# Kernel optimization log

Hardware: AMD Instinct MI355X
Metric: run time of the kernel (lower is better)

The kernel has to match this reference:

```python
import jax, jax.numpy as jnp
import numpy as np
from jax import lax

H = 1028  # hidden_size


def _lstm_layer(x, w_ih, w_hh, b_ih, b_hh):
    # x: [B, T, in], w_ih: [4H, in], w_hh: [4H, H] (PyTorch gate order i,f,g,o)
    B, T, _ = x.shape
    h_dim = w_hh.shape[1]
    # Precompute input contribution for all timesteps (memory-bound GEMM)
    xg = jnp.einsum('bti,gi->btg', x, w_ih) + b_ih + b_hh  # [B, T, 4H]

    def step(carry, xt):
        h, c = carry
        g = xt + h @ w_hh.T  # [B, 4H]
        i, f, gg, o = jnp.split(g, 4, axis=-1)
        i = jax.nn.sigmoid(i)
        f = jax.nn.sigmoid(f)
        gg = jnp.tanh(gg)
        o = jax.nn.sigmoid(o)
        c = f * c + i * gg
        h = o * jnp.tanh(c)
        return (h, c), h

    h0 = jnp.zeros((B, h_dim), x.dtype)
    c0 = jnp.zeros((B, h_dim), x.dtype)
    _, hs = lax.scan(step, (h0, c0), jnp.swapaxes(xg, 0, 1))  # [T, B, H]
    return jnp.swapaxes(hs, 0, 1)  # [B, T, H]


def setup_inputs() -> dict:
    key = jax.random.key(0)
    ks = jax.random.split(key, 12)
    s = 1.0 / np.sqrt(H)  # torch LSTM/Linear init scale

    def u(k, shape):
        return jax.random.uniform(k, shape, jnp.float32, -s, s)

    x = jax.random.normal(ks[0], (1, 16384, 1), dtype=jnp.float32)
    return {
        'x': x,
        'w_ih0': u(ks[1], (4 * H, 1)),
        'w_hh0': u(ks[2], (4 * H, H)),
        'b_ih0': u(ks[3], (4 * H,)),
        'b_hh0': u(ks[4], (4 * H,)),
        'w_ih1': u(ks[5], (4 * H, H)),
        'w_hh1': u(ks[6], (4 * H, H)),
        'b_ih1': u(ks[7], (4 * H,)),
        'b_hh1': u(ks[8], (4 * H,)),
        'lin_w': u(ks[9], (1, H)),
        'lin_b': u(ks[10], (1,)),
    }


def reference(x, w_ih0, w_hh0, b_ih0, b_hh0, w_ih1, w_hh1, b_ih1, b_hh1, lin_w, lin_b):
    h1 = _lstm_layer(x, w_ih0, w_hh0, b_ih0, b_hh0)   # [B, T, H]
    h2 = _lstm_layer(h1, w_ih1, w_hh1, b_ih1, b_hh1)  # [B, T, H]
    return h2 @ lin_w.T + lin_b                        # [B, T, 1]
```

## Files before the change

kernel.cpp:

```cpp
#include <hip/hip_runtime.h>
#include <math.h>

#define HH    1028
#define TT    16384
#define UP    1056
#define HSU   1056
#define HS    1056
#define NWG0  66
#define NWG1  132
#define NWGT  (NWG0 + NWG1)
#define R0    1024
#define R0M   (R0 - 1)
#define R1M   15

typedef unsigned long long u64;
typedef unsigned int uint4v __attribute__((ext_vector_type(4)));

__device__ __forceinline__ u64 ld_u64(const u64* p) {
    return __hip_atomic_load(p, __ATOMIC_RELAXED, __HIP_MEMORY_SCOPE_AGENT);
}
__device__ __forceinline__ void st_u64(u64* p, u64 v) {
    __hip_atomic_store(p, v, __ATOMIC_RELAXED, __HIP_MEMORY_SCOPE_AGENT);
}
__device__ __forceinline__ unsigned ld_u32(const unsigned* p) {
    return __hip_atomic_load(p, __ATOMIC_RELAXED, __HIP_MEMORY_SCOPE_AGENT);
}
__device__ __forceinline__ void st_u32(unsigned* p, unsigned v) {
    __hip_atomic_store(p, v, __ATOMIC_RELAXED, __HIP_MEMORY_SCOPE_AGENT);
}
__device__ __forceinline__ float sigmf(float x) { return 1.0f / (1.0f + expf(-x)); }
__device__ __forceinline__ u64 pack(unsigned tag, float v) {
    return ((u64)tag << 32) | (u64)__float_as_uint(v);
}

#define POLL16(dst, ptr) \
    asm volatile("global_load_dwordx4 %0, %1, off sc0 sc1" : "=v"(dst) : "v"(ptr))

__device__ __forceinline__ void stage132w(const u64* __restrict__ src, float* __restrict__ lds,
                                          int base, int lane, unsigned want, long long& budget) {
    const u64* p0 = src + base + 2 * lane;
    const u64* p1 = src + base + 2 * (64 + lane);
    bool d0 = false, d1 = (lane >= 2);
    uint4v r0 = {0, 0, 0, 0}, r1 = {0, 0, 0, 0};
    int spin = 2;
    for (;;) {
        if (!d0) POLL16(r0, p0);
        if (!d1) POLL16(r1, p1);
        asm volatile("s_waitcnt vmcnt(0)" ::: "memory");
        __builtin_amdgcn_sched_barrier(0);
        if (!d0 && r0[1] == want && r0[3] == want) {
            *(float2*)&lds[base + 2 * lane] =
                make_float2(__uint_as_float(r0[0]), __uint_as_float(r0[2]));
            d0 = true;
        }
        if (!d1 && r1[1] == want && r1[3] == want) {
            *(float2*)&lds[base + 2 * (64 + lane)] =
                make_float2(__uint_as_float(r1[0]), __uint_as_float(r1[2]));
            d1 = true;
        }
        if (__all(d0 & d1)) break;
        if (--budget < 0) break;
        if (spin > 0) { --spin; continue; }
        __builtin_amdgcn_s_sleep(1);
    }
}

__device__ __forceinline__ void stage264w(const u64* __restrict__ src, float* __restrict__ lds,
                                          int base, int lane, unsigned want, long long& budget) {
    const u64* p0 = src + base + 2 * lane;
    const u64* p1 = src + base + 2 * (64 + lane);
    const u64* p2 = src + base + 2 * (128 + lane);
    bool d0 = false, d1 = false, d2 = (lane >= 4);
    uint4v r0 = {0, 0, 0, 0}, r1 = {0, 0, 0, 0}, r2 = {0, 0, 0, 0};
    int spin = 2;
    for (;;) {
        if (!d0) POLL16(r0, p0);
        if (!d1) POLL16(r1, p1);
        if (!d2) POLL16(r2, p2);
        asm volatile("s_waitcnt vmcnt(0)" ::: "memory");
        __builtin_amdgcn_sched_barrier(0);
        if (!d0 && r0[1] == want && r0[3] == want) {
            *(float2*)&lds[base + 2 * lane] =
                make_float2(__uint_as_float(r0[0]), __uint_as_float(r0[2]));
            d0 = true;
        }
        if (!d1 && r1[1] == want && r1[3] == want) {
            *(float2*)&lds[base + 2 * (64 + lane)] =
                make_float2(__uint_as_float(r1[0]), __uint_as_float(r1[2]));
            d1 = true;
        }
        if (!d2 && r2[1] == want && r2[3] == want) {
            *(float2*)&lds[base + 2 * (128 + lane)] =
                make_float2(__uint_as_float(r2[0]), __uint_as_float(r2[2]));
            d2 = true;
        }
        if (__all(d0 & d1 & d2)) break;
        if (--budget < 0) break;
        if (spin > 0) { --spin; continue; }
        __builtin_amdgcn_s_sleep(1);
    }
}

__global__ __launch_bounds__(1024, 4) void wn_fused(
    const float* __restrict__ x,
    const float* __restrict__ w_ih0, const float* __restrict__ w_hh0,
    const float* __restrict__ b_ih0, const float* __restrict__ b_hh0,
    const float* __restrict__ w_ih1, const float* __restrict__ w_hh1,
    const float* __restrict__ b_ih1, const float* __restrict__ b_hh1,
    u64* __restrict__ ring0,
    u64* __restrict__ ring1,
    float* __restrict__ h2hist,
    unsigned* __restrict__ l1prog)
{
    __shared__ float smem[4 * UP + 128];
    const int tid  = threadIdx.x;
    const int lane = tid & 63;
    const int w    = tid >> 6;

    for (int i = tid; i < 4 * UP + 128; i += 1024) smem[i] = 0.0f;

    if (blockIdx.x < NWG0) {
        float* hbuf = smem;
        float* gbuf = smem + 2 * UP;
        const int wg   = blockIdx.x;
        const int row  = tid >> 4;
        const int k0   = tid & 15;
        const int gate = row >> 4;
        const int du   = row & 15;
        const int u    = wg * 16 + du;
        const bool real = (u < HH);
        const int wr   = gate * HH + (real ? u : 0);

        float wv[16][4], wt0 = 0.f, wt1 = 0.f;
#pragma unroll
        for (int m = 0; m < 16; ++m) {
            const int j = k0 * 4 + m * 64;
#pragma unroll
            for (int q = 0; q < 4; ++q)
                wv[m][q] = (real && j + q < HH) ? w_hh0[(size_t)wr * HH + j + q] : 0.0f;
        }
        {   const int j = 1024 + k0 * 2;
            wt0 = (real && j     < HH) ? w_hh0[(size_t)wr * HH + j]     : 0.0f;
            wt1 = (real && j + 1 < HH) ? w_hh0[(size_t)wr * HH + j + 1] : 0.0f; }
#pragma unroll
        for (int m = 0; m < 16; ++m)
#pragma unroll
            for (int q = 0; q < 4; ++q) asm volatile("" : "+v"(wv[m][q]));
        asm volatile("" : "+v"(wt0), "+v"(wt1));

        const float wx = real ? w_ih0[wr] : 0.0f;
        const float bs = real ? (b_ih0[wr] + b_hh0[wr]) : 0.0f;
        __syncthreads();

        long long budget = 20000000LL;
        float c_reg = 0.0f;
        for (int t = 0; t < TT; ++t) {
            if (t > 0) {
                if (w == 0) {
                    const float* gl = gbuf + ((t - 1) & 1) * 64;
                    if (lane < 16) {
                        const float gi = gl[lane], gf = gl[16 + lane];
                        const float gg = gl[32 + lane], go = gl[48 + lane];
                        const float iv = sigmf(gi), fv = sigmf(gf), gv = tanhf(gg), ov = sigmf(go);
                        c_reg = fv * c_reg + iv * gv;
                        float hv = ov * tanhf(c_reg);
                        if (wg * 16 + lane >= HH) hv = 0.0f;
                        st_u64(ring0 + (size_t)((t - 1) & R0M) * HSU + wg * 16 + lane,
                               pack((unsigned)t, hv));
                    }
                } else if (w >= 4 && w < 12) {
                    stage132w(ring0 + (size_t)((t - 1) & R0M) * HSU, hbuf + (t & 1) * UP,
                              (w - 4) * 132, lane, (unsigned)t, budget);
                } else if (w == 1 && lane == 0 && (t & 255) == 0) {
                    for (;;) {
                        unsigned p = ld_u32(l1prog);
                        if ((int)t - (int)p < R0 - 256) break;
                        if (--budget < 0) break;
                        __builtin_amdgcn_s_sleep(32);
                    }
                }
            }
            __syncthreads();
            const float* hb = hbuf + (t & 1) * UP;
            float acc = 0.0f;
#pragma unroll
            for (int m = 0; m < 16; ++m) {
                const float4 hv = *(const float4*)&hb[k0 * 4 + m * 64];
                acc = fmaf(wv[m][0], hv.x, acc);
                acc = fmaf(wv[m][1], hv.y, acc);
                acc = fmaf(wv[m][2], hv.z, acc);
                acc = fmaf(wv[m][3], hv.w, acc);
            }
            {   const float2 hv = *(const float2*)&hb[1024 + k0 * 2];
                acc = fmaf(wt0, hv.x, acc);
                acc = fmaf(wt1, hv.y, acc); }
#pragma unroll
            for (int off = 1; off < 16; off <<= 1) acc += __shfl_xor(acc, off);
            if (k0 == 0) gbuf[(t & 1) * 64 + row] = acc + x[t] * wx + bs;
            __syncthreads();
        }
        if (w == 0 && lane < 16) {
            const float* gl = gbuf + ((TT - 1) & 1) * 64;
            const float gi = gl[lane], gf = gl[16 + lane];
            const float gg = gl[32 + lane], go = gl[48 + lane];
            const float iv = sigmf(gi), fv = sigmf(gf), gv = tanhf(gg), ov = sigmf(go);
            c_reg = fv * c_reg + iv * gv;
            float hv = ov * tanhf(c_reg);
            if (wg * 16 + lane >= HH) hv = 0.0f;
            st_u64(ring0 + (size_t)((TT - 1) & R0M) * HSU + wg * 16 + lane,
                   pack((unsigned)TT, hv));
        }
    } else {
        float* abuf = smem;
        float* bbuf = smem + 2 * UP;
        float* gbuf = smem + 4 * UP;
        const int wg   = blockIdx.x - NWG0;
        const int row  = tid >> 5;
        const int k0   = tid & 31;
        const int gate = row >> 3;
        const int du   = row & 7;
        const int u    = wg * 8 + du;
        const bool real = (u < HH);
        const int wr   = gate * HH + (real ? u : 0);

        float wiv[8][4], whv[8][4], wit = 0.f, wht = 0.f;
#pragma unroll
        for (int m = 0; m < 8; ++m) {
            const int j = k0 * 4 + m * 128;
#pragma unroll
            for (int q = 0; q < 4; ++q) {
                const bool inb = real && (j + q < HH);
                wiv[m][q] = inb ? w_ih1[(size_t)wr * HH + j + q] : 0.0f;
                whv[m][q] = inb ? w_hh1[(size_t)wr * HH + j + q] : 0.0f;
            }
        }
        {   const int j = 1024 + k0;
            wit = (real && j < HH) ? w_ih1[(size_t)wr * HH + j] : 0.0f;
            wht = (real && j < HH) ? w_hh1[(size_t)wr * HH + j] : 0.0f; }
#pragma unroll
        for (int m = 0; m < 8; ++m)
#pragma unroll
            for (int q = 0; q < 4; ++q) {
                asm volatile("" : "+v"(wiv[m][q]));
                asm volatile("" : "+v"(whv[m][q]));
            }
        asm volatile("" : "+v"(wit), "+v"(wht));
        const float bs = real ? (b_ih1[wr] + b_hh1[wr]) : 0.0f;
        __syncthreads();

        long long budget = 20000000LL;
        float c_reg = 0.0f;
        for (int t = 0; t < TT; ++t) {
            if (w == 0) {
                if (t > 0) {
                    const float* gl = gbuf + ((t - 1) & 1) * 32;
                    if (lane < 8) {
                        const float gi = gl[lane], gf = gl[8 + lane];
                        const float gg = gl[16 + lane], go = gl[24 + lane];
                        const float iv = sigmf(gi), fv = sigmf(gf), gv = tanhf(gg), ov = sigmf(go);
                        c_reg = fv * c_reg + iv * gv;
                        float hv = ov * tanhf(c_reg);
                        if (wg * 8 + lane >= HH) hv = 0.0f;
                        st_u64(ring1 + (size_t)((t - 1) & R1M) * HSU + wg * 8 + lane,
                               pack((unsigned)t, hv));
                        h2hist[(size_t)(t - 1) * HS + wg * 8 + lane] = hv;
                    }
                }
            } else if (w >= 4 && w < 12) {
                if (t > 0)
                    stage132w(ring1 + (size_t)((t - 1) & R1M) * HSU, bbuf + (t & 1) * UP,
                              (w - 4) * 132, lane, (unsigned)t, budget);
            } else if (w >= 12) {
                stage264w(ring0 + (size_t)(t & R0M) * HSU, abuf + (t & 1) * UP,
                          (w - 12) * 264, lane, (unsigned)(t + 1), budget);
            }
            __syncthreads();
            const float* ab = abuf + (t & 1) * UP;
            const float* bb = bbuf + (t & 1) * UP;
            float acc = 0.0f;
#pragma unroll
            for (int m = 0; m < 8; ++m) {
                const float4 ha = *(const float4*)&ab[k0 * 4 + m * 128];
                const float4 hb2 = *(const float4*)&bb[k0 * 4 + m * 128];
                acc = fmaf(wiv[m][0], ha.x, acc);
                acc = fmaf(wiv[m][1], ha.y, acc);
                acc = fmaf(wiv[m][2], ha.z, acc);
                acc = fmaf(wiv[m][3], ha.w, acc);
                acc = fmaf(whv[m][0], hb2.x, acc);
                acc = fmaf(whv[m][1], hb2.y, acc);
                acc = fmaf(whv[m][2], hb2.z, acc);
                acc = fmaf(whv[m][3], hb2.w, acc);
            }
            acc = fmaf(wit, ab[1024 + k0], acc);
            acc = fmaf(wht, bb[1024 + k0], acc);
#pragma unroll
            for (int off = 1; off < 32; off <<= 1) acc += __shfl_xor(acc, off);
            if (k0 == 0) gbuf[(t & 1) * 32 + row] = acc + bs;
            __syncthreads();
            if (w == 1 && lane == 0 && wg == 0 && (t & 255) == 255)
                st_u32(l1prog, (unsigned)(t + 1));
        }
        if (w == 0 && lane < 8) {
            const float* gl = gbuf + ((TT - 1) & 1) * 32;
            const float gi = gl[lane], gf = gl[8 + lane];
            const float gg = gl[16 + lane], go = gl[24 + lane];
            const float iv = sigmf(gi), fv = sigmf(gf), gv = tanhf(gg), ov = sigmf(go);
            c_reg = fv * c_reg + iv * gv;
            float hv = ov * tanhf(c_reg);
            if (wg * 8 + lane >= HH) hv = 0.0f;
            h2hist[(size_t)(TT - 1) * HS + wg * 8 + lane] = hv;
        }
    }
}

__global__ __launch_bounds__(256) void wn_proj(
    const float* __restrict__ h2,
    const float* __restrict__ lin_w,
    const float* __restrict__ lin_b,
    float* __restrict__ out)
{
    const int lane = threadIdx.x & 63;
    const int wv   = threadIdx.x >> 6;
    const int t    = blockIdx.x * 4 + wv;
    const float* hp = h2 + (size_t)t * HS;
    float acc = 0.0f;
#pragma unroll
    for (int m = 0; m < 4; ++m) {
        const int j = lane * 4 + m * 256;
        const float4 h4 = *(const float4*)(hp + j);
        const float4 w4 = *(const float4*)(lin_w + j);
        acc += h4.x * w4.x + h4.y * w4.y + h4.z * w4.z + h4.w * w4.w;
    }
    if (lane == 0) {
#pragma unroll
        for (int j = 1024; j < HH; ++j) acc += hp[j] * lin_w[j];
    }
#pragma unroll
    for (int off = 1; off < 64; off <<= 1) acc += __shfl_xor(acc, off);
    if (lane == 0) out[t] = acc + lin_b[0];
}

extern "C" void kernel_launch(void* const* d_in, const int* in_sizes, int n_in,
                              void* d_out, int out_size, void* d_ws, size_t ws_size,
                              hipStream_t stream) {
    const float* x     = (const float*)d_in[0];
    const float* w_ih0 = (const float*)d_in[1];
    const float* w_hh0 = (const float*)d_in[2];
    const float* b_ih0 = (const float*)d_in[3];
    const float* b_hh0 = (const float*)d_in[4];
    const float* w_ih1 = (const float*)d_in[5];
    const float* w_hh1 = (const float*)d_in[6];
    const float* b_ih1 = (const float*)d_in[7];
    const float* b_hh1 = (const float*)d_in[8];
    const float* lin_w = (const float*)d_in[9];
    const float* lin_b = (const float*)d_in[10];
    float* out = (float*)d_out;

    char* ws = (char*)d_ws;
    const size_t R0B = (size_t)R0 * HSU * 8;
    const size_t R1B = (size_t)16 * HSU * 8;
    const size_t H2B = (size_t)TT * HS * 4;
    u64* ring0 = (u64*)(ws);
    u64* ring1 = (u64*)(ws + R0B);
    float* h2hist = (float*)(ws + R0B + R1B);
    unsigned* l1prog = (unsigned*)(ws + R0B + R1B + H2B);

    wn_fused<<<NWGT, 1024, 0, stream>>>(x, w_ih0, w_hh0, b_ih0, b_hh0,
                                        w_ih1, w_hh1, b_ih1, b_hh1,
                                        ring0, ring1, h2hist, l1prog);
    wn_proj<<<TT / 4, 256, 0, stream>>>(h2hist, lin_w, lin_b, out);
}
```

Before: 42.34 ms.

## Give each wave one hidden unit, compute gates in-wave, cut per-step barriers

Restructures both LSTM layers so each wave owns one hidden unit and holds all four gate rows of weights in registers. The wave reduces its dot products with a full-wave shuffle and applies the gate nonlinearities itself, which removes the separate gate buffer and the second barrier per timestep. Per-unit results are packed with a step tag into LDS slots and collected by wave 0, which publishes them to the global ring. Every wave then helps poll the next step's hidden state, so the loop needs one __syncthreads per step instead of two. The cost is more weight registers per lane, a full 64-lane shuffle reduction per gate, and an LDS spin-wait on the critical path.

```diff
diff --git a/kernel.cpp b/kernel.cpp
--- a/kernel.cpp
+++ b/kernel.cpp
@@ -28,6 +28,12 @@
 __device__ __forceinline__ void st_u32(unsigned* p, unsigned v) {
     __hip_atomic_store(p, v, __ATOMIC_RELAXED, __HIP_MEMORY_SCOPE_AGENT);
 }
+__device__ __forceinline__ u64 ld_lds_u64(const u64* p) {
+    return __hip_atomic_load(p, __ATOMIC_RELAXED, __HIP_MEMORY_SCOPE_WORKGROUP);
+}
+__device__ __forceinline__ void st_lds_u64(u64* p, u64 v) {
+    __hip_atomic_store(p, v, __ATOMIC_RELAXED, __HIP_MEMORY_SCOPE_WORKGROUP);
+}
 __device__ __forceinline__ float sigmf(float x) { return 1.0f / (1.0f + expf(-x)); }
 __device__ __forceinline__ u64 pack(unsigned tag, float v) {
     return ((u64)tag << 32) | (u64)__float_as_uint(v);
@@ -36,16 +42,14 @@
 #define POLL16(dst, ptr) \
     asm volatile("global_load_dwordx4 %0, %1, off sc0 sc1" : "=v"(dst) : "v"(ptr))
 
-__device__ __forceinline__ void stage132w(const u64* __restrict__ src, float* __restrict__ lds,
-                                          int base, int lane, unsigned want, long long& budget) {
+__device__ __forceinline__ void stage66w(const u64* __restrict__ src, float* __restrict__ lds,
+                                         int base, int lane, unsigned want, long long& budget) {
     const u64* p0 = src + base + 2 * lane;
-    const u64* p1 = src + base + 2 * (64 + lane);
-    bool d0 = false, d1 = (lane >= 2);
-    uint4v r0 = {0, 0, 0, 0}, r1 = {0, 0, 0, 0};
+    bool d0 = (lane >= 33);
+    uint4v r0 = {0, 0, 0, 0};
     int spin = 2;
     for (;;) {
         if (!d0) POLL16(r0, p0);
-        if (!d1) POLL16(r1, p1);
         asm volatile("s_waitcnt vmcnt(0)" ::: "memory");
         __builtin_amdgcn_sched_barrier(0);
         if (!d0 && r0[1] == want && r0[3] == want) {
@@ -53,12 +57,7 @@
                 make_float2(__uint_as_float(r0[0]), __uint_as_float(r0[2]));
             d0 = true;
         }
-        if (!d1 && r1[1] == want && r1[3] == want) {
-            *(float2*)&lds[base + 2 * (64 + lane)] =
-                make_float2(__uint_as_float(r1[0]), __uint_as_float(r1[2]));
-            d1 = true;
-        }
-        if (__all(d0 & d1)) break;
+        if (__all(d0)) break;
         if (--budget < 0) break;
         if (spin > 0) { --spin; continue; }
         __builtin_amdgcn_s_sleep(1);
@@ -112,203 +111,239 @@
     float* __restrict__ h2hist,
     unsigned* __restrict__ l1prog)
 {
-    __shared__ float smem[4 * UP + 128];
+    __shared__ float smem[4 * UP + 64];
     const int tid  = threadIdx.x;
     const int lane = tid & 63;
     const int w    = tid >> 6;
 
-    for (int i = tid; i < 4 * UP + 128; i += 1024) smem[i] = 0.0f;
+    for (int i = tid; i < 4 * UP + 64; i += 1024) smem[i] = 0.0f;
 
     if (blockIdx.x < NWG0) {
         float* hbuf = smem;
-        float* gbuf = smem + 2 * UP;
+        u64*   pbuf = (u64*)(smem + 4 * UP);
         const int wg   = blockIdx.x;
-        const int row  = tid >> 4;
-        const int k0   = tid & 15;
-        const int gate = row >> 4;
-        const int du   = row & 15;
-        const int u    = wg * 16 + du;
+        const int u    = wg * 16 + w;
         const bool real = (u < HH);
-        const int wr   = gate * HH + (real ? u : 0);
-
-        float wv[16][4], wt0 = 0.f, wt1 = 0.f;
-#pragma unroll
-        for (int m = 0; m < 16; ++m) {
-            const int j = k0 * 4 + m * 64;
-#pragma unroll
-            for (int q = 0; q < 4; ++q)
-                wv[m][q] = (real && j + q < HH) ? w_hh0[(size_t)wr * HH + j + q] : 0.0f;
-        }
-        {   const int j = 1024 + k0 * 2;
-            wt0 = (real && j     < HH) ? w_hh0[(size_t)wr * HH + j]     : 0.0f;
-            wt1 = (real && j + 1 < HH) ? w_hh0[(size_t)wr * HH + j + 1] : 0.0f; }
-#pragma unroll
-        for (int m = 0; m < 16; ++m)
-#pragma unroll
-            for (int q = 0; q < 4; ++q) asm volatile("" : "+v"(wv[m][q]));
-        asm volatile("" : "+v"(wt0), "+v"(wt1));
-
-        const float wx = real ? w_ih0[wr] : 0.0f;
-        const float bs = real ? (b_ih0[wr] + b_hh0[wr]) : 0.0f;
+
+        float wv[4][4][4];
+        float wt[4][4];
+        float wx[4], bsg[4];
+#pragma unroll
+        for (int g = 0; g < 4; ++g) {
+            const int wr = g * HH + (real ? u : 0);
+#pragma unroll
+            for (int m = 0; m < 4; ++m) {
+                const int j = lane * 4 + m * 256;
+#pragma unroll
+                for (int q = 0; q < 4; ++q)
+                    wv[g][m][q] = real ? w_hh0[(size_t)wr * HH + j + q] : 0.0f;
+            }
+#pragma unroll
+            for (int q = 0; q < 4; ++q) {
+                const int j = 1024 + lane * 4 + q;
+                wt[g][q] = (real && lane < 8 && j < HH) ? w_hh0[(size_t)wr * HH + j] : 0.0f;
+            }
+            wx[g]  = real ? w_ih0[wr] : 0.0f;
+            bsg[g] = real ? (b_ih0[wr] + b_hh0[wr]) : 0.0f;
+        }
+#pragma unroll
+        for (int g = 0; g < 4; ++g)
+#pragma unroll
+            for (int m = 0; m < 4; ++m)
+#pragma unroll
+                for (int q = 0; q < 4; ++q) asm volatile("" : "+v"(wv[g][m][q]));
         __syncthreads();
 
         long long budget = 20000000LL;
         float c_reg = 0.0f;
         for (int t = 0; t < TT; ++t) {
-            if (t > 0) {
-                if (w == 0) {
-                    const float* gl = gbuf + ((t - 1) & 1) * 64;
-                    if (lane < 16) {
-                        const float gi = gl[lane], gf = gl[16 + lane];
-                        const float gg = gl[32 + lane], go = gl[48 + lane];
-                        const float iv = sigmf(gi), fv = sigmf(gf), gv = tanhf(gg), ov = sigmf(go);
-                        c_reg = fv * c_reg + iv * gv;
-                        float hv = ov * tanhf(c_reg);
-                        if (wg * 16 + lane >= HH) hv = 0.0f;
-                        st_u64(ring0 + (size_t)((t - 1) & R0M) * HSU + wg * 16 + lane,
-                               pack((unsigned)t, hv));
-                    }
-                } else if (w >= 4 && w < 12) {
-                    stage132w(ring0 + (size_t)((t - 1) & R0M) * HSU, hbuf + (t & 1) * UP,
-                              (w - 4) * 132, lane, (unsigned)t, budget);
-                } else if (w == 1 && lane == 0 && (t & 255) == 0) {
-                    for (;;) {
-                        unsigned p = ld_u32(l1prog);
-                        if ((int)t - (int)p < R0 - 256) break;
-                        if (--budget < 0) break;
-                        __builtin_amdgcn_s_sleep(32);
-                    }
-                }
-            }
-            __syncthreads();
+            const float xt = x[t];
             const float* hb = hbuf + (t & 1) * UP;
-            float acc = 0.0f;
-#pragma unroll
-            for (int m = 0; m < 16; ++m) {
-                const float4 hv = *(const float4*)&hb[k0 * 4 + m * 64];
-                acc = fmaf(wv[m][0], hv.x, acc);
-                acc = fmaf(wv[m][1], hv.y, acc);
-                acc = fmaf(wv[m][2], hv.z, acc);
-                acc = fmaf(wv[m][3], hv.w, acc);
-            }
-            {   const float2 hv = *(const float2*)&hb[1024 + k0 * 2];
-                acc = fmaf(wt0, hv.x, acc);
-                acc = fmaf(wt1, hv.y, acc); }
-#pragma unroll
-            for (int off = 1; off < 16; off <<= 1) acc += __shfl_xor(acc, off);
-            if (k0 == 0) gbuf[(t & 1) * 64 + row] = acc + x[t] * wx + bs;
-            __syncthreads();
-        }
-        if (w == 0 && lane < 16) {
-            const float* gl = gbuf + ((TT - 1) & 1) * 64;
-            const float gi = gl[lane], gf = gl[16 + lane];
-            const float gg = gl[32 + lane], go = gl[48 + lane];
-            const float iv = sigmf(gi), fv = sigmf(gf), gv = tanhf(gg), ov = sigmf(go);
+            float acc[4] = {0.f, 0.f, 0.f, 0.f};
+#pragma unroll
+            for (int m = 0; m < 4; ++m) {
+                const float4 hv4 = *(const float4*)&hb[lane * 4 + m * 256];
+#pragma unroll
+                for (int g = 0; g < 4; ++g) {
+                    acc[g] = fmaf(wv[g][m][0], hv4.x, acc[g]);
+                    acc[g] = fmaf(wv[g][m][1], hv4.y, acc[g]);
+                    acc[g] = fmaf(wv[g][m][2], hv4.z, acc[g]);
+                    acc[g] = fmaf(wv[g][m][3], hv4.w, acc[g]);
+                }
+            }
+            if (lane < 8) {
+                const float4 hv4 = *(const float4*)&hb[1024 + lane * 4];
+#pragma unroll
+                for (int g = 0; g < 4; ++g) {
+                    acc[g] = fmaf(wt[g][0], hv4.x, acc[g]);
+                    acc[g] = fmaf(wt[g][1], hv4.y, acc[g]);
+                    acc[g] = fmaf(wt[g][2], hv4.z, acc[g]);
+                    acc[g] = fmaf(wt[g][3], hv4.w, acc[g]);
+                }
+            }
+#pragma unroll
+            for (int off = 1; off < 64; off <<= 1) {
+#pragma unroll
+                for (int g = 0; g < 4; ++g) acc[g] += __shfl_xor(acc[g], off);
+            }
+#pragma unroll
+            for (int g = 0; g < 4; ++g) acc[g] = fmaf(xt, wx[g], acc[g]) + bsg[g];
+            const float iv = sigmf(acc[0]), fv = sigmf(acc[1]);
+            const float gv = tanhf(acc[2]), ov = sigmf(acc[3]);
             c_reg = fv * c_reg + iv * gv;
             float hv = ov * tanhf(c_reg);
-            if (wg * 16 + lane >= HH) hv = 0.0f;
-            st_u64(ring0 + (size_t)((TT - 1) & R0M) * HSU + wg * 16 + lane,
-                   pack((unsigned)TT, hv));
+            if (!real) hv = 0.0f;
+            if (lane == 0) st_lds_u64(&pbuf[w], pack((unsigned)(t + 1), hv));
+
+            if (w == 0) {
+                const unsigned want = (unsigned)(t + 1);
+                u64 pv = 0; bool d = (lane >= 16);
+                for (;;) {
+                    if (!d) { u64 v2 = ld_lds_u64(&pbuf[lane]);
+                              if ((unsigned)(v2 >> 32) == want) { pv = v2; d = true; } }
+                    if (__all(d)) break;
+                    if (--budget < 0) break;
+                }
+                if (lane < 16)
+                    st_u64(ring0 + (size_t)(t & R0M) * HSU + wg * 16 + lane, pv);
+            } else if (w == 1 && lane == 0 && t > 0 && (t & 255) == 0) {
+                for (;;) {
+                    unsigned p = ld_u32(l1prog);
+                    if ((int)t - (int)p < R0 - 256) break;
+                    if (--budget < 0) break;
+                    __builtin_amdgcn_s_sleep(32);
+                }
+            }
+            if (t + 1 < TT)
+                stage66w(ring0 + (size_t)(t & R0M) * HSU, hbuf + ((t + 1) & 1) * UP,
+                         w * 66, lane, (unsigned)(t + 1), budget);
+            __syncthreads();
         }
     } else {
         float* abuf = smem;
         float* bbuf = smem + 2 * UP;
-        float* gbuf = smem + 4 * UP;
+        u64*   pbuf = (u64*)(smem + 4 * UP);
         const int wg   = blockIdx.x - NWG0;
-        const int row  = tid >> 5;
-        const int k0   = tid & 31;
-        const int gate = row >> 3;
-        const int du   = row & 7;
-        const int u    = wg * 8 + du;
-        const bool real = (u < HH);
-        const int wr   = gate * HH + (real ? u : 0);
-
-        float wiv[8][4], whv[8][4], wit = 0.f, wht = 0.f;
-#pragma unroll
-        for (int m = 0; m < 8; ++m) {
-            const int j = k0 * 4 + m * 128;
-#pragma unroll
-            for (int q = 0; q < 4; ++q) {
-                const bool inb = real && (j + q < HH);
-                wiv[m][q] = inb ? w_ih1[(size_t)wr * HH + j + q] : 0.0f;
-                whv[m][q] = inb ? w_hh1[(size_t)wr * HH + j + q] : 0.0f;
-            }
-        }
-        {   const int j = 1024 + k0;
-            wit = (real && j < HH) ? w_ih1[(size_t)wr * HH + j] : 0.0f;
-            wht = (real && j < HH) ? w_hh1[(size_t)wr * HH + j] : 0.0f; }
-#pragma unroll
-        for (int m = 0; m < 8; ++m)
-#pragma unroll
-            for (int q = 0; q < 4; ++q) {
-                asm volatile("" : "+v"(wiv[m][q]));
-                asm volatile("" : "+v"(whv[m][q]));
-            }
-        asm volatile("" : "+v"(wit), "+v"(wht));
-        const float bs = real ? (b_ih1[wr] + b_hh1[wr]) : 0.0f;
+        const bool comp = (w < 8);
+        const int u    = wg * 8 + (comp ? w : 0);
+        const bool real = comp && (u < HH);
+
+        float wiv[4][4][4], whv[4][4][4];
+        float wti[4][4], wth[4][4], bsg[4];
+        if (comp) {
+#pragma unroll
+            for (int g = 0; g < 4; ++g) {
+                const int wr = g * HH + (real ? u : 0);
+#pragma unroll
+                for (int m = 0; m < 4; ++m) {
+                    const int j = lane * 4 + m * 256;
+#pragma unroll
+                    for (int q = 0; q < 4; ++q) {
+                        wiv[g][m][q] = real ? w_ih1[(size_t)wr * HH + j + q] : 0.0f;
+                        whv[g][m][q] = real ? w_hh1[(size_t)wr * HH + j + q] : 0.0f;
+                    }
+                }
+#pragma unroll
+                for (int q = 0; q < 4; ++q) {
+                    const int j = 1024 + lane * 4 + q;
+                    const bool inb = real && lane < 8 && j < HH;
+                    wti[g][q] = inb ? w_ih1[(size_t)wr * HH + j] : 0.0f;
+                    wth[g][q] = inb ? w_hh1[(size_t)wr * HH + j] : 0.0f;
+                }
+                bsg[g] = real ? (b_ih1[wr] + b_hh1[wr]) : 0.0f;
+            }
+#pragma unroll
+            for (int g = 0; g < 4; ++g)
+#pragma unroll
+                for (int m = 0; m < 4; ++m)
+#pragma unroll
+                    for (int q = 0; q < 4; ++q) {
+                        asm volatile("" : "+v"(wiv[g][m][q]));
+                        asm volatile("" : "+v"(whv[g][m][q]));
+                    }
+        }
+        long long budget = 20000000LL;
+        if (w >= 12)
+            stage264w(ring0, abuf, (w - 12) * 264, lane, 1u, budget);
         __syncthreads();
 
-        long long budget = 20000000LL;
         float c_reg = 0.0f;
         for (int t = 0; t < TT; ++t) {
-            if (w == 0) {
-                if (t > 0) {
-                    const float* gl = gbuf + ((t - 1) & 1) * 32;
+            if (comp) {
+                const float* ab = abuf + (t & 1) * UP;
+                const float* bb = bbuf + (t & 1) * UP;
+                float acc[4] = {0.f, 0.f, 0.f, 0.f};
+#pragma unroll
+                for (int m = 0; m < 4; ++m) {
+                    const float4 ha = *(const float4*)&ab[lane * 4 + m * 256];
+                    const float4 hc = *(const float4*)&bb[lane * 4 + m * 256];
+#pragma unroll
+                    for (int g = 0; g < 4; ++g) {
+                        acc[g] = fmaf(wiv[g][m][0], ha.x, acc[g]);
+                        acc[g] = fmaf(wiv[g][m][1], ha.y, acc[g]);
+                        acc[g] = fmaf(wiv[g][m][2], ha.z, acc[g]);
+                        acc[g] = fmaf(wiv[g][m][3], ha.w, acc[g]);
+                        acc[g] = fmaf(whv[g][m][0], hc.x, acc[g]);
+                        acc[g] = fmaf(whv[g][m][1], hc.y, acc[g]);
+                        acc[g] = fmaf(whv[g][m][2], hc.z, acc[g]);
+                        acc[g] = fmaf(whv[g][m][3], hc.w, acc[g]);
+                    }
+                }
+                if (lane < 8) {
+                    const float4 ha = *(const float4*)&ab[1024 + lane * 4];
+                    const float4 hc = *(const float4*)&bb[1024 + lane * 4];
+#pragma unroll
+                    for (int g = 0; g < 4; ++g) {
+                        acc[g] = fmaf(wti[g][0], ha.x, acc[g]);
+                        acc[g] = fmaf(wti[g][1], ha.y, acc[g]);
+                        acc[g] = fmaf(wti[g][2], ha.z, acc[g]);
+                        acc[g] = fmaf(wti[g][3], ha.w, acc[g]);
+                        acc[g] = fmaf(wth[g][0], hc.x, acc[g]);
+                        acc[g] = fmaf(wth[g][1], hc.y, acc[g]);
+                        acc[g] = fmaf(wth[g][2], hc.z, acc[g]);
+                        acc[g] = fmaf(wth[g][3], hc.w, acc[g]);
+                    }
+                }
+#pragma unroll
+                for (int off = 1; off < 64; off <<= 1) {
+#pragma unroll
+                    for (int g = 0; g < 4; ++g) acc[g] += __shfl_xor(acc[g], off);
+                }
+#pragma unroll
+                for (int g = 0; g < 4; ++g) acc[g] += bsg[g];
+                const float iv = sigmf(acc[0]), fv = sigmf(acc[1]);
+                const float gv = tanhf(acc[2]), ov = sigmf(acc[3]);
+                c_reg = fv * c_reg + iv * gv;
+                float hv = ov * tanhf(c_reg);
+                if (!real) hv = 0.0f;
+                if (lane == 0) st_lds_u64(&pbuf[w], pack((unsigned)(t + 1), hv));
+
+                if (w == 0) {
+                    const unsigned want = (unsigned)(t + 1);
+                    u64 pv = 0; bool d = (lane >= 8);
+                    for (;;) {
+                        if (!d) { u64 v2 = ld_lds_u64(&pbuf[lane]);
+                                  if ((unsigned)(v2 >> 32) == want) { pv = v2; d = true; } }
+                        if (__all(d)) break;
+                        if (--budget < 0) break;
+                    }
                     if (lane < 8) {
-                        const float gi = gl[lane], gf = gl[8 + lane];
-                        const float gg = gl[16 + lane], go = gl[24 + lane];
-                        const float iv = sigmf(gi), fv = sigmf(gf), gv = tanhf(gg), ov = sigmf(go);
-                        c_reg = fv * c_reg + iv * gv;
-                        float hv = ov * tanhf(c_reg);
-                        if (wg * 8 + lane >= HH) hv = 0.0f;
-                        st_u64(ring1 + (size_t)((t - 1) & R1M) * HSU + wg * 8 + lane,
-                               pack((unsigned)t, hv));
-                        h2hist[(size_t)(t - 1) * HS + wg * 8 + lane] = hv;
-                    }
-                }
-            } else if (w >= 4 && w < 12) {
-                if (t > 0)
-                    stage132w(ring1 + (size_t)((t - 1) & R1M) * HSU, bbuf + (t & 1) * UP,
-                              (w - 4) * 132, lane, (unsigned)t, budget);
-            } else if (w >= 12) {
-                stage264w(ring0 + (size_t)(t & R0M) * HSU, abuf + (t & 1) * UP,
-                          (w - 12) * 264, lane, (unsigned)(t + 1), budget);
+                        st_u64(ring1 + (size_t)(t & R1M) * HSU + wg * 8 + lane, pv);
+                        h2hist[(size_t)t * HS + wg * 8 + lane] = __uint_as_float((unsigned)pv);
+                    }
+                } else if (wg == 0 && w == 1 && lane == 0 && (t & 255) == 255) {
+                    st_u32(l1prog, (unsigned)(t + 1));
+                }
+            } else if (w < 12) {
+                if (t + 1 < TT)
+                    stage264w(ring1 + (size_t)(t & R1M) * HSU, bbuf + ((t + 1) & 1) * UP,
+                              (w - 8) * 264, lane, (unsigned)(t + 1), budget);
+            } else {
+                if (t + 1 < TT)
+                    stage264w(ring0 + (size_t)((t + 1) & R0M) * HSU, abuf + ((t + 1) & 1) * UP,
+                              (w - 12) * 264, lane, (unsigned)(t + 2), budget);
             }
             __syncthreads();
-            const float* ab = abuf + (t & 1) * UP;
-            const float* bb = bbuf + (t & 1) * UP;
-            float acc = 0.0f;
-#pragma unroll
-            for (int m = 0; m < 8; ++m) {
-                const float4 ha = *(const float4*)&ab[k0 * 4 + m * 128];
-                const float4 hb2 = *(const float4*)&bb[k0 * 4 + m * 128];
-                acc = fmaf(wiv[m][0], ha.x, acc);
-                acc = fmaf(wiv[m][1], ha.y, acc);
-                acc = fmaf(wiv[m][2], ha.z, acc);
-                acc = fmaf(wiv[m][3], ha.w, acc);
-                acc = fmaf(whv[m][0], hb2.x, acc);
-                acc = fmaf(whv[m][1], hb2.y, acc);
-                acc = fmaf(whv[m][2], hb2.z, acc);
-                acc = fmaf(whv[m][3], hb2.w, acc);
-            }
-            acc = fmaf(wit, ab[1024 + k0], acc);
-            acc = fmaf(wht, bb[1024 + k0], acc);
-#pragma unroll
-            for (int off = 1; off < 32; off <<= 1) acc += __shfl_xor(acc, off);
-            if (k0 == 0) gbuf[(t & 1) * 32 + row] = acc + bs;
-            __syncthreads();
-            if (w == 1 && lane == 0 && wg == 0 && (t & 255) == 255)
-                st_u32(l1prog, (unsigned)(t + 1));
-        }
-        if (w == 0 && lane < 8) {
-            const float* gl = gbuf + ((TT - 1) & 1) * 32;
-            const float gi = gl[lane], gf = gl[8 + lane];
-            const float gg = gl[16 + lane], go = gl[24 + lane];
-            const float iv = sigmf(gi), fv = sigmf(gf), gv = tanhf(gg), ov = sigmf(go);
-            c_reg = fv * c_reg + iv * gv;
-            float hv = ov * tanhf(c_reg);
-            if (wg * 8 + lane >= HH) hv = 0.0f;
-            h2hist[(size_t)(TT - 1) * HS + wg * 8 + lane] = hv;
         }
     }
 }
```

Result: slower. 144.1 ms (+240.4%).

## Halve workgroup size and have each thread compute all four gates of one unit

Applied to the files above, without the earlier changes.

Each workgroup now runs 512 threads instead of 1024. Each thread holds the weights for all four gates of one hidden unit and reuses every loaded h vector across four accumulators. This cuts the number of waves per workgroup and the LDS reads per FMA, which should shorten the per-timestep critical path through __syncthreads. Staging from the rings is spread over fewer, wider waves (176/352 elements each). The cost is more registers per thread, and each wave now has fewer pollers and a longer shuffle reduction.

```diff
diff --git a/kernel.cpp b/kernel.cpp
--- a/kernel.cpp
+++ b/kernel.cpp
@@ -36,11 +36,11 @@
 #define POLL16(dst, ptr) \
     asm volatile("global_load_dwordx4 %0, %1, off sc0 sc1" : "=v"(dst) : "v"(ptr))
 
-__device__ __forceinline__ void stage132w(const u64* __restrict__ src, float* __restrict__ lds,
+__device__ __forceinline__ void stage176w(const u64* __restrict__ src, float* __restrict__ lds,
                                           int base, int lane, unsigned want, long long& budget) {
     const u64* p0 = src + base + 2 * lane;
     const u64* p1 = src + base + 2 * (64 + lane);
-    bool d0 = false, d1 = (lane >= 2);
+    bool d0 = false, d1 = (lane >= 24);
     uint4v r0 = {0, 0, 0, 0}, r1 = {0, 0, 0, 0};
     int spin = 2;
     for (;;) {
@@ -65,12 +65,12 @@
     }
 }
 
-__device__ __forceinline__ void stage264w(const u64* __restrict__ src, float* __restrict__ lds,
+__device__ __forceinline__ void stage352w(const u64* __restrict__ src, float* __restrict__ lds,
                                           int base, int lane, unsigned want, long long& budget) {
     const u64* p0 = src + base + 2 * lane;
     const u64* p1 = src + base + 2 * (64 + lane);
     const u64* p2 = src + base + 2 * (128 + lane);
-    bool d0 = false, d1 = false, d2 = (lane >= 4);
+    bool d0 = false, d1 = false, d2 = (lane >= 48);
     uint4v r0 = {0, 0, 0, 0}, r1 = {0, 0, 0, 0}, r2 = {0, 0, 0, 0};
     int spin = 2;
     for (;;) {
@@ -101,7 +101,7 @@
     }
 }
 
-__global__ __launch_bounds__(1024, 4) void wn_fused(
+__global__ __launch_bounds__(512, 2) void wn_fused(
     const float* __restrict__ x,
     const float* __restrict__ w_ih0, const float* __restrict__ w_hh0,
     const float* __restrict__ b_ih0, const float* __restrict__ b_hh0,
@@ -117,39 +117,40 @@
     const int lane = tid & 63;
     const int w    = tid >> 6;
 
-    for (int i = tid; i < 4 * UP + 128; i += 1024) smem[i] = 0.0f;
+    for (int i = tid; i < 4 * UP + 128; i += 512) smem[i] = 0.0f;
 
     if (blockIdx.x < NWG0) {
         float* hbuf = smem;
         float* gbuf = smem + 2 * UP;
         const int wg   = blockIdx.x;
-        const int row  = tid >> 4;
-        const int k0   = tid & 15;
-        const int gate = row >> 4;
-        const int du   = row & 15;
+        const int hi   = lane >> 5;
+        const int k0   = lane & 31;
+        const int du   = w * 2 + hi;
         const int u    = wg * 16 + du;
         const bool real = (u < HH);
-        const int wr   = gate * HH + (real ? u : 0);
-
-        float wv[16][4], wt0 = 0.f, wt1 = 0.f;
-#pragma unroll
-        for (int m = 0; m < 16; ++m) {
-            const int j = k0 * 4 + m * 64;
-#pragma unroll
-            for (int q = 0; q < 4; ++q)
-                wv[m][q] = (real && j + q < HH) ? w_hh0[(size_t)wr * HH + j + q] : 0.0f;
-        }
-        {   const int j = 1024 + k0 * 2;
-            wt0 = (real && j     < HH) ? w_hh0[(size_t)wr * HH + j]     : 0.0f;
-            wt1 = (real && j + 1 < HH) ? w_hh0[(size_t)wr * HH + j + 1] : 0.0f; }
-#pragma unroll
-        for (int m = 0; m < 16; ++m)
-#pragma unroll
-            for (int q = 0; q < 4; ++q) asm volatile("" : "+v"(wv[m][q]));
-        asm volatile("" : "+v"(wt0), "+v"(wt1));
-
-        const float wx = real ? w_ih0[wr] : 0.0f;
-        const float bs = real ? (b_ih0[wr] + b_hh0[wr]) : 0.0f;
+
+        float wv[4][8][4], wt4[4], wx4[4], bs4[4];
+#pragma unroll
+        for (int g = 0; g < 4; ++g) {
+            const int wr = g * HH + (real ? u : 0);
+#pragma unroll
+            for (int m = 0; m < 8; ++m) {
+                const int j = k0 * 4 + m * 128;
+#pragma unroll
+                for (int q = 0; q < 4; ++q)
+                    wv[g][m][q] = real ? w_hh0[(size_t)wr * HH + j + q] : 0.0f;
+            }
+            const int jt = 1024 + k0;
+            wt4[g] = (real && jt < HH) ? w_hh0[(size_t)wr * HH + jt] : 0.0f;
+            wx4[g] = real ? w_ih0[wr] : 0.0f;
+            bs4[g] = real ? (b_ih0[wr] + b_hh0[wr]) : 0.0f;
+        }
+#pragma unroll
+        for (int g = 0; g < 4; ++g)
+#pragma unroll
+            for (int m = 0; m < 8; ++m)
+#pragma unroll
+                for (int q = 0; q < 4; ++q) asm volatile("" : "+v"(wv[g][m][q]));
         __syncthreads();
 
         long long budget = 20000000LL;
@@ -168,9 +169,9 @@
                         st_u64(ring0 + (size_t)((t - 1) & R0M) * HSU + wg * 16 + lane,
                                pack((unsigned)t, hv));
                     }
-                } else if (w >= 4 && w < 12) {
-                    stage132w(ring0 + (size_t)((t - 1) & R0M) * HSU, hbuf + (t & 1) * UP,
-                              (w - 4) * 132, lane, (unsigned)t, budget);
+                } else if (w >= 2) {
+                    stage176w(ring0 + (size_t)((t - 1) & R0M) * HSU, hbuf + (t & 1) * UP,
+                              (w - 2) * 176, lane, (unsigned)t, budget);
                 } else if (w == 1 && lane == 0 && (t & 255) == 0) {
                     for (;;) {
                         unsigned p = ld_u32(l1prog);
@@ -182,21 +183,33 @@
             }
             __syncthreads();
             const float* hb = hbuf + (t & 1) * UP;
-            float acc = 0.0f;
-#pragma unroll
-            for (int m = 0; m < 16; ++m) {
-                const float4 hv = *(const float4*)&hb[k0 * 4 + m * 64];
-                acc = fmaf(wv[m][0], hv.x, acc);
-                acc = fmaf(wv[m][1], hv.y, acc);
-                acc = fmaf(wv[m][2], hv.z, acc);
-                acc = fmaf(wv[m][3], hv.w, acc);
-            }
-            {   const float2 hv = *(const float2*)&hb[1024 + k0 * 2];
-                acc = fmaf(wt0, hv.x, acc);
-                acc = fmaf(wt1, hv.y, acc); }
-#pragma unroll
-            for (int off = 1; off < 16; off <<= 1) acc += __shfl_xor(acc, off);
-            if (k0 == 0) gbuf[(t & 1) * 64 + row] = acc + x[t] * wx + bs;
+            float acc[4] = {0.f, 0.f, 0.f, 0.f};
+#pragma unroll
+            for (int m = 0; m < 8; ++m) {
+                const float4 hv4 = *(const float4*)&hb[k0 * 4 + m * 128];
+#pragma unroll
+                for (int g = 0; g < 4; ++g) {
+                    acc[g] = fmaf(wv[g][m][0], hv4.x, acc[g]);
+                    acc[g] = fmaf(wv[g][m][1], hv4.y, acc[g]);
+                    acc[g] = fmaf(wv[g][m][2], hv4.z, acc[g]);
+                    acc[g] = fmaf(wv[g][m][3], hv4.w, acc[g]);
+                }
+            }
+            {   const float ht = hb[1024 + k0];
+#pragma unroll
+                for (int g = 0; g < 4; ++g) acc[g] = fmaf(wt4[g], ht, acc[g]); }
+#pragma unroll
+            for (int off = 1; off < 32; off <<= 1) {
+#pragma unroll
+                for (int g = 0; g < 4; ++g) acc[g] += __shfl_xor(acc[g], off);
+            }
+            if (k0 == 0) {
+                const float xt = x[t];
+                float* gw = gbuf + (t & 1) * 64;
+#pragma unroll
+                for (int g = 0; g < 4; ++g)
+                    gw[g * 16 + du] = fmaf(xt, wx4[g], acc[g]) + bs4[g];
+            }
             __syncthreads();
         }
         if (w == 0 && lane < 16) {
@@ -215,37 +228,38 @@
         float* bbuf = smem + 2 * UP;
         float* gbuf = smem + 4 * UP;
         const int wg   = blockIdx.x - NWG0;
-        const int row  = tid >> 5;
-        const int k0   = tid & 31;
-        const int gate = row >> 3;
-        const int du   = row & 7;
+        const int du   = w;
         const int u    = wg * 8 + du;
         const bool real = (u < HH);
-        const int wr   = gate * HH + (real ? u : 0);
-
-        float wiv[8][4], whv[8][4], wit = 0.f, wht = 0.f;
-#pragma unroll
-        for (int m = 0; m < 8; ++m) {
-            const int j = k0 * 4 + m * 128;
-#pragma unroll
-            for (int q = 0; q < 4; ++q) {
-                const bool inb = real && (j + q < HH);
-                wiv[m][q] = inb ? w_ih1[(size_t)wr * HH + j + q] : 0.0f;
-                whv[m][q] = inb ? w_hh1[(size_t)wr * HH + j + q] : 0.0f;
-            }
-        }
-        {   const int j = 1024 + k0;
-            wit = (real && j < HH) ? w_ih1[(size_t)wr * HH + j] : 0.0f;
-            wht = (real && j < HH) ? w_hh1[(size_t)wr * HH + j] : 0.0f; }
-#pragma unroll
-        for (int m = 0; m < 8; ++m)
-#pragma unroll
-            for (int q = 0; q < 4; ++q) {
-                asm volatile("" : "+v"(wiv[m][q]));
-                asm volatile("" : "+v"(whv[m][q]));
-            }
-        asm volatile("" : "+v"(wit), "+v"(wht));
-        const float bs = real ? (b_ih1[wr] + b_hh1[wr]) : 0.0f;
+
+        float wiv[4][4][4], whv[4][4][4], wti4[4], wth4[4], bs4[4];
+#pragma unroll
+        for (int g = 0; g < 4; ++g) {
+            const int wr = g * HH + (real ? u : 0);
+#pragma unroll
+            for (int m = 0; m < 4; ++m) {
+                const int j = lane * 4 + m * 256;
+#pragma unroll
+                for (int q = 0; q < 4; ++q) {
+                    wiv[g][m][q] = real ? w_ih1[(size_t)wr * HH + j + q] : 0.0f;
+                    whv[g][m][q] = real ? w_hh1[(size_t)wr * HH + j + q] : 0.0f;
+                }
+            }
+            const int jt = 1024 + lane;
+            const bool inb = real && lane < 32 && jt < HH;
+            wti4[g] = inb ? w_ih1[(size_t)wr * HH + jt] : 0.0f;
+            wth4[g] = inb ? w_hh1[(size_t)wr * HH + jt] : 0.0f;
+            bs4[g]  = real ? (b_ih1[wr] + b_hh1[wr]) : 0.0f;
+        }
+#pragma unroll
+        for (int g = 0; g < 4; ++g)
+#pragma unroll
+            for (int m = 0; m < 4; ++m)
+#pragma unroll
+                for (int q = 0; q < 4; ++q) {
+                    asm volatile("" : "+v"(wiv[g][m][q]));
+                    asm volatile("" : "+v"(whv[g][m][q]));
+                }
         __syncthreads();
 
         long long budget = 20000000LL;
@@ -266,36 +280,53 @@
                         h2hist[(size_t)(t - 1) * HS + wg * 8 + lane] = hv;
                     }
                 }
-            } else if (w >= 4 && w < 12) {
+            } else if (w >= 2 && w < 5) {
                 if (t > 0)
-                    stage132w(ring1 + (size_t)((t - 1) & R1M) * HSU, bbuf + (t & 1) * UP,
-                              (w - 4) * 132, lane, (unsigned)t, budget);
-            } else if (w >= 12) {
-                stage264w(ring0 + (size_t)(t & R0M) * HSU, abuf + (t & 1) * UP,
-                          (w - 12) * 264, lane, (unsigned)(t + 1), budget);
+                    stage352w(ring1 + (size_t)((t - 1) & R1M) * HSU, bbuf + (t & 1) * UP,
+                              (w - 2) * 352, lane, (unsigned)t, budget);
+            } else if (w >= 5) {
+                stage352w(ring0 + (size_t)(t & R0M) * HSU, abuf + (t & 1) * UP,
+                          (w - 5) * 352, lane, (unsigned)(t + 1), budget);
             }
             __syncthreads();
             const float* ab = abuf + (t & 1) * UP;
             const float* bb = bbuf + (t & 1) * UP;
-            float acc = 0.0f;
-#pragma unroll
-            for (int m = 0; m < 8; ++m) {
-                const float4 ha = *(const float4*)&ab[k0 * 4 + m * 128];
-                const float4 hb2 = *(const float4*)&bb[k0 * 4 + m * 128];
-                acc = fmaf(wiv[m][0], ha.x, acc);
-                acc = fmaf(wiv[m][1], ha.y, acc);
-                acc = fmaf(wiv[m][2], ha.z, acc);
-                acc = fmaf(wiv[m][3], ha.w, acc);
-                acc = fmaf(whv[m][0], hb2.x, acc);
-                acc = fmaf(whv[m][1], hb2.y, acc);
-                acc = fmaf(whv[m][2], hb2.z, acc);
-                acc = fmaf(whv[m][3], hb2.w, acc);
-            }
-            acc = fmaf(wit, ab[1024 + k0], acc);
-            acc = fmaf(wht, bb[1024 + k0], acc);
-#pragma unroll
-            for (int off = 1; off < 32; off <<= 1) acc += __shfl_xor(acc, off);
-            if (k0 == 0) gbuf[(t & 1) * 32 + row] = acc + bs;
+            float acc[4] = {0.f, 0.f, 0.f, 0.f};
+#pragma unroll
+            for (int m = 0; m < 4; ++m) {
+                const float4 ha = *(const float4*)&ab[lane * 4 + m * 256];
+                const float4 hc = *(const float4*)&bb[lane * 4 + m * 256];
+#pragma unroll
+                for (int g = 0; g < 4; ++g) {
+                    acc[g] = fmaf(wiv[g][m][0], ha.x, acc[g]);
+                    acc[g] = fmaf(wiv[g][m][1], ha.y, acc[g]);
+                    acc[g] = fmaf(wiv[g][m][2], ha.z, acc[g]);
+                    acc[g] = fmaf(wiv[g][m][3], ha.w, acc[g]);
+                    acc[g] = fmaf(whv[g][m][0], hc.x, acc[g]);
+                    acc[g] = fmaf(whv[g][m][1], hc.y, acc[g]);
+                    acc[g] = fmaf(whv[g][m][2], hc.z, acc[g]);
+                    acc[g] = fmaf(whv[g][m][3], hc.w, acc[g]);
+                }
+            }
+            if (lane < 32) {
+                const float ha = ab[1024 + lane];
+                const float hc = bb[1024 + lane];
+#pragma unroll
+                for (int g = 0; g < 4; ++g) {
+                    acc[g] = fmaf(wti4[g], ha, acc[g]);
+                    acc[g] = fmaf(wth4[g], hc, acc[g]);
+                }
+            }
+#pragma unroll
+            for (int off = 1; off < 64; off <<= 1) {
+#pragma unroll
+                for (int g = 0; g < 4; ++g) acc[g] += __shfl_xor(acc[g], off);
+            }
+            if (lane == 0) {
+                float* gw = gbuf + (t & 1) * 32;
+#pragma unroll
+                for (int g = 0; g < 4; ++g) gw[g * 8 + du] = acc[g] + bs4[g];
+            }
             __syncthreads();
             if (w == 1 && lane == 0 && wg == 0 && (t & 255) == 255)
                 st_u32(l1prog, (unsigned)(t + 1));
@@ -365,8 +396,8 @@
     float* h2hist = (float*)(ws + R0B + R1B);
     unsigned* l1prog = (unsigned*)(ws + R0B + R1B + H2B);
 
-    wn_fused<<<NWGT, 1024, 0, stream>>>(x, w_ih0, w_hh0, b_ih0, b_hh0,
-                                        w_ih1, w_hh1, b_ih1, b_hh1,
-                                        ring0, ring1, h2hist, l1prog);
+    wn_fused<<<NWGT, 512, 0, stream>>>(x, w_ih0, w_hh0, b_ih0, b_hh0,
+                                       w_ih1, w_hh1, b_ih1, b_hh1,
+                                       ring0, ring1, h2hist, l1prog);
     wn_proj<<<TT / 4, 256, 0, stream>>>(h2hist, lin_w, lin_b, out);
 }
```

After: 45.34 ms. +7.1%, slower.
